# Optimization experiments

Measured on AMD Instinct MI355X. Metric: run time of the kernel, lower is better.

## Reference

```python
import jax, jax.numpy as jnp
import numpy as np
import math

GROUPS = 32
EPS = 1e-5

def group_norm(x, w, b):
    B, C, H, W = x.shape
    xg = x.reshape(B, GROUPS, C // GROUPS, H, W)
    mu = xg.mean(axis=(2, 3, 4), keepdims=True)
    var = xg.var(axis=(2, 3, 4), keepdims=True)
    xn = ((xg - mu) * jax.lax.rsqrt(var + EPS)).reshape(B, C, H, W)
    return xn * w[None, :, None, None] + b[None, :, None, None]

def conv1x1(x, w, b):
    # x: [B,Cin,H,W], w: [Cout,Cin], b: [Cout]
    return jnp.einsum('bchw,oc->bohw', x, w) + b[None, :, None, None]

def setup_inputs() -> dict:
    key = jax.random.key(0)
    ks = jax.random.split(key, 8)
    B, C, E, H, W = 8, 256, 512, 64, 64
    x = jax.random.normal(ks[0], (B, C, H, W), dtype=jnp.float32)
    condA = jax.random.normal(ks[1], (B, E, H, W), dtype=jnp.float32)
    gn_x_w = jnp.ones((C,), jnp.float32)
    gn_x_b = jnp.zeros((C,), jnp.float32)
    gn_c_w = jnp.ones((E,), jnp.float32)
    gn_c_b = jnp.zeros((E,), jnp.float32)
    q_w = jax.random.normal(ks[2], (C, C), jnp.float32) * 0.02
    q_b = jnp.zeros((C,), jnp.float32)
    k_w = jax.random.normal(ks[3], (C, E), jnp.float32) * 0.02
    k_b = jnp.zeros((C,), jnp.float32)
    v_w = jax.random.normal(ks[4], (C, E), jnp.float32) * 0.02
    v_b = jnp.zeros((C,), jnp.float32)
    return {"x": x, "condA": condA, "gn_x_w": gn_x_w, "gn_x_b": gn_x_b,
            "gn_c_w": gn_c_w, "gn_c_b": gn_c_b, "q_w": q_w, "q_b": q_b,
            "k_w": k_w, "k_b": k_b, "v_w": v_w, "v_b": v_b}

def reference(x, condA, gn_x_w, gn_x_b, gn_c_w, gn_c_b, q_w, q_b, k_w, k_b, v_w, v_b):
    B, C, H, W = x.shape
    scale = math.sqrt(C)
    h = group_norm(x, gn_x_w, gn_x_b)
    h1 = group_norm(condA, gn_c_w, gn_c_b)
    q = conv1x1(h, q_w, q_b)      # [B,C,H,W]
    k = conv1x1(h1, k_w, k_b)     # [B,C,Hc,Wc]
    v = conv1x1(h1, v_w, v_b)     # [B,C,Hc,Wc]
    qf = q.transpose(0, 2, 3, 1).reshape(B, H * W, C)        # [B,N,C]
    kf = k.reshape(B, C, -1)                                  # [B,C,M]
    vf = v.transpose(0, 2, 3, 1).reshape(B, -1, C)            # [B,M,C]
    attn = jax.nn.softmax(jnp.einsum('bnc,bcm->bnm', qf, kf) / scale, axis=-1)
    out = jnp.einsum('bnm,bmc->bnc', attn, vf)                # [B,N,C]
    return out.reshape(B, H, W, C).transpose(0, 3, 1, 2)
```

## Files before the change

### kernel.cpp

```cpp
#include <hip/hip_runtime.h>


typedef _Float16 half8 __attribute__((ext_vector_type(8)));
typedef _Float16 half4v __attribute__((ext_vector_type(4)));
typedef float f32x4 __attribute__((ext_vector_type(4)));
typedef float f32x16 __attribute__((ext_vector_type(16)));

#define MFMA16(a, b, c) __builtin_amdgcn_mfma_f32_16x16x32_f16((a), (b), (c), 0, 0, 0)
#define MFMA32(a, b, c) __builtin_amdgcn_mfma_f32_32x32x16_f16((a), (b), (c), 0, 0, 0)

__global__ __launch_bounds__(256) void statswconv_kernel(
    const float* __restrict__ x, const float* __restrict__ condA,
    float* __restrict__ sx, float* __restrict__ sc,
    const float* __restrict__ wq, const float* __restrict__ wk,
    const float* __restrict__ wv, _Float16* __restrict__ wqt,
    _Float16* __restrict__ wkt, _Float16* __restrict__ wvt) {
  int bid = blockIdx.x;
  int t = threadIdx.x;
  if (bid >= 512) {
    int i = (bid - 512) * 256 + t;
    const float* src;
    _Float16* dst;
    int cin, ksbits, gi;
    if (i < 8192) { src = wq; dst = wqt; cin = 256; ksbits = 3; gi = i; }
    else if (i < 24576) { src = wk; dst = wkt; cin = 512; ksbits = 4; gi = i - 8192; }
    else { src = wv; dst = wvt; cin = 512; ksbits = 4; gi = i - 24576; }
    int tile = gi >> 6, g = gi & 63;
    int otile = tile >> ksbits, ks = tile & ((1 << ksbits) - 1);
    int o = otile * 16 + (g & 15), k = ks * 32 + (g >> 4) * 8;
    const float* s = src + (size_t)o * cin + k;
    half8 hv;
#pragma unroll
    for (int j = 0; j < 8; j++) hv[j] = (_Float16)s[j];
    *(half8*)(dst + (size_t)gi * 8) = hv;
    return;
  }
  const float4* src;
  int nf4;
  float* dst;
  float inv_n;
  if (bid < 256) {
    src = (const float4*)(x + (size_t)bid * 32768);
    nf4 = 8192;
    dst = sx + bid * 2;
    inv_n = 1.0f / 32768.0f;
  } else {
    int j = bid - 256;
    src = (const float4*)(condA + (size_t)j * 65536);
    nf4 = 16384;
    dst = sc + j * 2;
    inv_n = 1.0f / 65536.0f;
  }
  float s = 0.f, s2 = 0.f;
  for (int i = t; i < nf4; i += 256) {
    float4 v = src[i];
    s += v.x + v.y + v.z + v.w;
    s2 += v.x * v.x + v.y * v.y + v.z * v.z + v.w * v.w;
  }
#pragma unroll
  for (int m = 1; m <= 32; m <<= 1) {
    s += __shfl_xor(s, m, 64);
    s2 += __shfl_xor(s2, m, 64);
  }
  __shared__ float red[8];
  int w = t >> 6;
  if ((t & 63) == 0) { red[w * 2] = s; red[w * 2 + 1] = s2; }
  __syncthreads();
  if (t == 0) {
    float S = red[0] + red[2] + red[4] + red[6];
    float S2 = red[1] + red[3] + red[5] + red[7];
    float mu = S * inv_n;
    float var = S2 * inv_n - mu * mu;
    dst[0] = mu;
    dst[1] = rsqrtf(var + 1e-5f);
  }
}

__global__ __launch_bounds__(256) void ntrans_kernel(
    const float* __restrict__ x, const float* __restrict__ condA,
    const float* __restrict__ statsx, const float* __restrict__ statsc,
    const float* __restrict__ gxw, const float* __restrict__ gxb,
    const float* __restrict__ gcw, const float* __restrict__ gcb,
    _Float16* __restrict__ hxTt, _Float16* __restrict__ h1Tt) {
  int bid = blockIdx.x;
  const float *src, *stats, *gw, *gb;
  _Float16* dst;
  int CH, gsh, bid2;
  if (bid < 2048) {
    src = x; stats = statsx; gw = gxw; gb = gxb; dst = hxTt;
    CH = 256; gsh = 3; bid2 = bid;
  } else {
    src = condA; stats = statsc; gw = gcw; gb = gcb; dst = h1Tt;
    CH = 512; gsh = 4; bid2 = bid - 2048;
  }
  int b = bid2 & 7, nt = (bid2 >> 3) & 63, ctile = bid2 >> 9;
  int n0 = nt * 64, c0 = ctile * 64;
  int t = threadIdx.x;
  __shared__ float tile[64][65];

  int cl = t >> 2;
  int c = c0 + cl;
  const float* st = stats + ((size_t)b * 32 + (c >> gsh)) * 2;
  float mu = st[0], rs = st[1];
  float a = rs * gw[c];
  float bb = gb[c] - mu * a;
  const float* srow = src + ((size_t)(b * CH + c)) * 4096 + n0 + (t & 3) * 16;
#pragma unroll
  for (int i = 0; i < 4; i++) {
    float4 v = *(const float4*)(srow + 4 * i);
    int nn = (t & 3) * 16 + 4 * i;
    tile[cl][nn + 0] = v.x * a + bb;
    tile[cl][nn + 1] = v.y * a + bb;
    tile[cl][nn + 2] = v.z * a + bb;
    tile[cl][nn + 3] = v.w * a + bb;
  }
  __syncthreads();
  int nl = t >> 2;
  half8 ov[2];
#pragma unroll
  for (int u = 0; u < 2; u++)
#pragma unroll
    for (int i = 0; i < 8; i++) ov[u][i] = (_Float16)tile[(t & 3) * 16 + 8 * u + i][nl];
  int n = n0 + nl;
  size_t tb = ((size_t)b * 256 + (n >> 4)) * (CH >> 5);
  int ca = c0 + (t & 3) * 16;
#pragma unroll
  for (int u = 0; u < 2; u++) {
    int cc = ca + 8 * u;
    size_t addr = ((tb + (cc >> 5)) * 64 + (n & 15) + 16 * ((cc >> 3) & 3)) * 8;
    *(half8*)(dst + addr) = ov[u];
  }
}

__global__ __launch_bounds__(256, 2) void projQ_kernel(
    const _Float16* __restrict__ Ht, const _Float16* __restrict__ Wt,
    const float* __restrict__ bias, _Float16* __restrict__ Qt) {
  int bid = blockIdx.x;
  int b = bid & 7, nt = bid >> 3;
  int t = threadIdx.x, l = t & 63, w = t >> 6;
  int c15 = l & 15, q = l >> 4;

  __shared__ __align__(16) _Float16 hbuf[16384];
  half8* hb = (half8*)hbuf;
  {
    const half8* sg = (const half8*)Ht + (size_t)(b * 256 + nt * 4) * 512;
#pragma unroll
    for (int i = 0; i < 8; i++) hb[t + 256 * i] = sg[t + 256 * i];
  }
  __syncthreads();

  const half8* wt8 = (const half8*)Wt;
#pragma unroll
  for (int p = 0; p < 2; p++) {
    int oa = (p * 4 + w) * 2;
    f32x4 acc[2][4] = {};
#pragma unroll
    for (int ks = 0; ks < 8; ks++) {
      half8 af0 = wt8[((size_t)(oa + 0) * 8 + ks) * 64 + l];
      half8 af1 = wt8[((size_t)(oa + 1) * 8 + ks) * 64 + l];
#pragma unroll
      for (int nt2 = 0; nt2 < 4; nt2++) {
        half8 bf = hb[(nt2 * 8 + ks) * 64 + l];
        acc[0][nt2] = MFMA16(af0, bf, acc[0][nt2]);
        acc[1][nt2] = MFMA16(af1, bf, acc[1][nt2]);
      }
    }
#pragma unroll
    for (int j = 0; j < 2; j++) {
      int o4 = (oa + j) * 16 + 4 * q;
      f32x4 bv = *(const f32x4*)(bias + o4);
#pragma unroll
      for (int nt2 = 0; nt2 < 4; nt2++) {
        half4v hv;
#pragma unroll
        for (int r = 0; r < 4; r++) hv[r] = (_Float16)((acc[j][nt2][r] + bv[r]) * 0.0625f);
        size_t addr = ((((size_t)b * 128 + nt * 2 + (nt2 >> 1)) * 16 + (oa + j)) * 64 +
                       (nt2 & 1) * 16 + c15 + 32 * (q >> 1)) * 8 + (q & 1) * 4;
        *(half4v*)(Qt + addr) = hv;
      }
    }
  }
}

__global__ __launch_bounds__(256, 2) void projKV_kernel(
    const _Float16* __restrict__ Ht, const _Float16* __restrict__ Wk,
    const _Float16* __restrict__ Wv, const float* __restrict__ kb,
    const float* __restrict__ vb, _Float16* __restrict__ Kt,
    _Float16* __restrict__ Vt) {
  int bid = blockIdx.x;
  int b = bid & 7, mt = bid >> 3;
  int m0 = mt * 64;
  int t = threadIdx.x, l = t & 63, w = t >> 6;
  int c15 = l & 15, q = l >> 4;

  __shared__ __align__(16) _Float16 hbuf[32768];
  half8* hb = (half8*)hbuf;
  {
    const half8* sg = (const half8*)Ht + (size_t)(b * 256 + mt * 4) * 1024;
#pragma unroll
    for (int i = 0; i < 16; i++) hb[t + 256 * i] = sg[t + 256 * i];
  }
  __syncthreads();

  const half8* wk8 = (const half8*)Wk;
  const half8* wv8 = (const half8*)Wv;
#pragma unroll
  for (int p = 0; p < 2; p++) {
    int oa = (p * 4 + w) * 2;
    f32x4 acck[2][4] = {};
    f32x4 accv[4][2] = {};
#pragma unroll
    for (int ks = 0; ks < 16; ks++) {
      half8 kf0 = wk8[((size_t)(oa + 0) * 16 + ks) * 64 + l];
      half8 kf1 = wk8[((size_t)(oa + 1) * 16 + ks) * 64 + l];
      half8 vf0 = wv8[((size_t)(oa + 0) * 16 + ks) * 64 + l];
      half8 vf1 = wv8[((size_t)(oa + 1) * 16 + ks) * 64 + l];
#pragma unroll
      for (int nt2 = 0; nt2 < 4; nt2++) {
        half8 lf = hb[(nt2 * 16 + ks) * 64 + l];
        acck[0][nt2] = MFMA16(kf0, lf, acck[0][nt2]);
        acck[1][nt2] = MFMA16(kf1, lf, acck[1][nt2]);
        accv[nt2][0] = MFMA16(lf, vf0, accv[nt2][0]);
        accv[nt2][1] = MFMA16(lf, vf1, accv[nt2][1]);
      }
    }
#pragma unroll
    for (int j = 0; j < 2; j++) {
      int o4 = (oa + j) * 16 + 4 * q;
      f32x4 bv = *(const f32x4*)(kb + o4);
#pragma unroll
      for (int nt2 = 0; nt2 < 4; nt2++) {
        half4v hv;
#pragma unroll
        for (int r = 0; r < 4; r++) hv[r] = (_Float16)(acck[j][nt2][r] + bv[r]);
        size_t addr = ((((size_t)b * 128 + mt * 2 + (nt2 >> 1)) * 16 + (oa + j)) * 64 +
                       (nt2 & 1) * 16 + c15 + 32 * (q >> 1)) * 8 + (q & 1) * 4;
        *(half4v*)(Kt + addr) = hv;
      }
    }
#pragma unroll
    for (int nt2 = 0; nt2 < 4; nt2++) {
      int m = m0 + nt2 * 16 + 4 * q;
      size_t mbase = ((size_t)b * 256 + (m >> 4)) * 8;
#pragma unroll
      for (int j = 0; j < 2; j++) {
        int c = (oa + j) * 16 + c15;
        float bs = vb[c];
        half4v hv;
#pragma unroll
        for (int r = 0; r < 4; r++) hv[r] = (_Float16)(accv[nt2][j][r] + bs);
        size_t addr = ((mbase + (c >> 5)) * 64 + (c & 31) + ((q >> 1) << 5)) * 8 + (q & 1) * 4;
        *(half4v*)(Vt + addr) = hv;
      }
    }
  }
}

__global__ __launch_bounds__(256, 2) void attn_kernel(
    const _Float16* __restrict__ Qt, const _Float16* __restrict__ Kt,
    const _Float16* __restrict__ Vt, float* __restrict__ out) {
  int bid = blockIdx.x;
  int b = bid & 7, nt = bid >> 3;
  int n0 = nt * 64;
  int t = threadIdx.x, l = t & 63, w = t >> 6;
  int l31 = l & 31, h = l >> 5;
  int mh = w & 1, nh = w >> 1;

  __shared__ __align__(16) _Float16 kbuf[16384];
  __shared__ __align__(16) _Float16 pbuf[4096];
  __shared__ float lsw[2][64];
  half8* kb8 = (half8*)kbuf;

  half8 qf[16];
  {
    const half8* qt8 = (const half8*)Qt + ((size_t)(b * 128 + nt * 2 + nh) * 16) * 64 + l;
#pragma unroll
    for (int ks = 0; ks < 16; ks++) qf[ks] = qt8[ks * 64];
  }

  const half8* ktb = (const half8*)Kt + (size_t)b * 131072 + t;
  const half8* vt8 = (const half8*)Vt + (size_t)b * 256 * 8 * 64;
  int gb = (l31 ^ h) | (h << 5);

  f32x16 acc_o[4] = {};
  float l_part = 0.f;

  half8 kreg[8];
#pragma unroll
  for (int i = 0; i < 8; i++) kreg[i] = ktb[256 * i];
#pragma unroll
  for (int i = 0; i < 8; i++) kb8[t + 256 * i] = kreg[i];
  __syncthreads();

  for (int it = 0; it < 64; it++) {
    int itn = it < 63 ? it + 1 : 63;
#pragma unroll
    for (int i = 0; i < 8; i++) kreg[i] = ktb[itn * 2048 + 256 * i];
    half8 vf0[8];
#pragma unroll
    for (int u = 0; u < 2; u++)
#pragma unroll
      for (int ct = 0; ct < 4; ct++)
        vf0[u * 4 + ct] = vt8[((size_t)(it * 4 + u) * 8 + (mh * 4 + ct)) * 64 + l];

    f32x16 s = {};
#pragma unroll
    for (int ks = 0; ks < 16; ks++) {
      half8 kf = kb8[(mh * 16 + ks) * 64 + l];
      s = MFMA32(kf, qf[ks], s);
    }

    half4v pv[4];
#pragma unroll
    for (int k2 = 0; k2 < 4; k2++) {
#pragma unroll
      for (int r = 0; r < 4; r++) {
        float e = __expf(s[4 * k2 + r]);
        l_part += e;
        pv[k2][r] = (_Float16)e;
      }
    }
    __syncthreads();

#pragma unroll
    for (int k2 = 0; k2 < 4; k2++) {
      int hm = k2 & 1;
      int tau = nh * 4 + mh * 2 + (k2 >> 1);
      int g = (l31 ^ hm) | (hm << 5);
      *(half4v*)&pbuf[tau * 512 + g * 8 + 4 * h] = pv[k2];
    }
#pragma unroll
    for (int i = 0; i < 8; i++) kb8[t + 256 * i] = kreg[i];
    __syncthreads();

    half8 vf1[8];
#pragma unroll
    for (int u = 0; u < 2; u++)
#pragma unroll
      for (int ct = 0; ct < 4; ct++)
        vf1[u * 4 + ct] = vt8[((size_t)(it * 4 + 2 + u) * 8 + (mh * 4 + ct)) * 64 + l];
#pragma unroll
    for (int ks = 0; ks < 2; ks++) {
      half8 pf = *(const half8*)&pbuf[(nh * 4 + ks) * 512 + gb * 8];
#pragma unroll
      for (int ct = 0; ct < 4; ct++) acc_o[ct] = MFMA32(pf, vf0[ks * 4 + ct], acc_o[ct]);
    }
#pragma unroll
    for (int ks = 2; ks < 4; ks++) {
      half8 pf = *(const half8*)&pbuf[(nh * 4 + ks) * 512 + gb * 8];
#pragma unroll
      for (int ct = 0; ct < 4; ct++) acc_o[ct] = MFMA32(pf, vf1[(ks - 2) * 4 + ct], acc_o[ct]);
    }
  }

  {
    float v = l_part + __shfl_xor(l_part, 32, 64);
    if (l < 32) lsw[mh][nh * 32 + l] = v;
  }
  __syncthreads();
#pragma unroll
  for (int k2 = 0; k2 < 4; k2++) {
    int nb = nh * 32 + 4 * h + 8 * k2;
    f32x4 s0 = *(const f32x4*)&lsw[0][nb];
    f32x4 s1 = *(const f32x4*)&lsw[1][nb];
    f32x4 linv;
#pragma unroll
    for (int r = 0; r < 4; r++) linv[r] = 1.0f / (s0[r] + s1[r]);
#pragma unroll
    for (int ct = 0; ct < 4; ct++) {
      int c = mh * 128 + ct * 32 + l31;
      f32x4 o4;
#pragma unroll
      for (int r = 0; r < 4; r++) o4[r] = acc_o[ct][4 * k2 + r] * linv[r];
      *(f32x4*)(out + ((size_t)(b * 256 + c)) * 4096 + n0 + nb) = o4;
    }
  }
}

extern "C" void kernel_launch(void* const* d_in, const int* in_sizes, int n_in,
                              void* d_out, int out_size, void* d_ws,
                              size_t ws_size, hipStream_t stream) {
  const float* x = (const float*)d_in[0];
  const float* condA = (const float*)d_in[1];
  const float* gxw = (const float*)d_in[2];
  const float* gxb = (const float*)d_in[3];
  const float* gcw = (const float*)d_in[4];
  const float* gcb = (const float*)d_in[5];
  const float* qw = (const float*)d_in[6];
  const float* qb = (const float*)d_in[7];
  const float* kw = (const float*)d_in[8];
  const float* kb = (const float*)d_in[9];
  const float* vw = (const float*)d_in[10];
  const float* vb = (const float*)d_in[11];
  float* out = (float*)d_out;

  char* ws = (char*)d_ws;
  float* statsx = (float*)(ws);
  float* statsc = (float*)(ws + 2048);
  _Float16* wqt = (_Float16*)(ws + 4096);
  _Float16* wkt = (_Float16*)(ws + 135168);
  _Float16* wvt = (_Float16*)(ws + 397312);
  char* p = ws + 659456;
  _Float16* hxTt = (_Float16*)p; p += (size_t)8 * 4096 * 256 * 2;
  _Float16* h1Tt = (_Float16*)p; p += (size_t)8 * 4096 * 512 * 2;
  _Float16* Qt = (_Float16*)p;   p += (size_t)8 * 4096 * 256 * 2;
  _Float16* Kt = (_Float16*)p;   p += (size_t)8 * 4096 * 256 * 2;
  _Float16* Vt = (_Float16*)p;

  statswconv_kernel<<<672, 256, 0, stream>>>(x, condA, statsx, statsc,
                                             qw, kw, vw, wqt, wkt, wvt);
  ntrans_kernel<<<6144, 256, 0, stream>>>(x, condA, statsx, statsc,
                                          gxw, gxb, gcw, gcb, hxTt, h1Tt);
  projQ_kernel<<<512, 256, 0, stream>>>(hxTt, wqt, qb, Qt);
  projKV_kernel<<<512, 256, 0, stream>>>(h1Tt, wkt, wvt, kb, vb, Kt, Vt);
  attn_kernel<<<512, 256, 0, stream>>>(Qt, Kt, Vt, out);
}
```

Baseline: 392.9 us.

## Split attention key range across two blocks and add a combine kernel

The attention kernel now splits the 4096 keys into two halves, so the grid grows from 512 to 1024 blocks. Each block writes unnormalized partial outputs and per-row softmax denominators, and a new combine kernel sums the two halves and divides. The goal is to fill the GPU better, since 512 blocks gave only two per CU; launch bounds are also raised to 4 blocks per CU. In exchange it adds partial-output writes, a combine pass that reads and writes again, and a risk of register spilling under the tighter register budget. The partials reuse workspace that the projection kernels have already consumed.

After: 1.224 ms. 211% more time.

```diff
diff --git a/kernel.cpp b/kernel.cpp
--- a/kernel.cpp
+++ b/kernel.cpp
@@ -256,19 +256,22 @@
   }
 }
 
-__global__ __launch_bounds__(256, 2) void attn_kernel(
+__global__ __launch_bounds__(256, 4) void attn_kernel(
     const _Float16* __restrict__ Qt, const _Float16* __restrict__ Kt,
-    const _Float16* __restrict__ Vt, float* __restrict__ out) {
+    const _Float16* __restrict__ Vt, float* __restrict__ out,
+    float* __restrict__ O1, float* __restrict__ l0g,
+    float* __restrict__ l1g) {
   int bid = blockIdx.x;
-  int b = bid & 7, nt = bid >> 3;
+  int b = bid & 7, nt = (bid >> 3) & 63, ms = bid >> 9;
   int n0 = nt * 64;
   int t = threadIdx.x, l = t & 63, w = t >> 6;
   int l31 = l & 31, h = l >> 5;
   int mh = w & 1, nh = w >> 1;
+  int it0 = ms * 32, it1 = it0 + 32;
 
   __shared__ __align__(16) _Float16 kbuf[16384];
   __shared__ __align__(16) _Float16 pbuf[4096];
-  __shared__ float lsw[2][64];
+  float* lsw = (float*)pbuf;
   half8* kb8 = (half8*)kbuf;
 
   half8 qf[16];
@@ -287,13 +290,13 @@
 
   half8 kreg[8];
 #pragma unroll
-  for (int i = 0; i < 8; i++) kreg[i] = ktb[256 * i];
+  for (int i = 0; i < 8; i++) kreg[i] = ktb[it0 * 2048 + 256 * i];
 #pragma unroll
   for (int i = 0; i < 8; i++) kb8[t + 256 * i] = kreg[i];
   __syncthreads();
 
-  for (int it = 0; it < 64; it++) {
-    int itn = it < 63 ? it + 1 : 63;
+  for (int it = it0; it < it1; it++) {
+    int itn = it + 1 < it1 ? it + 1 : it1 - 1;
 #pragma unroll
     for (int i = 0; i < 8; i++) kreg[i] = ktb[itn * 2048 + 256 * i];
     half8 vf0[8];
@@ -353,28 +356,45 @@
     }
   }
 
+  __syncthreads();
   {
     float v = l_part + __shfl_xor(l_part, 32, 64);
-    if (l < 32) lsw[mh][nh * 32 + l] = v;
-  }
-  __syncthreads();
+    if (l < 32) lsw[mh * 64 + nh * 32 + l] = v;
+  }
+  __syncthreads();
+  float* obase = ms ? O1 : out;
 #pragma unroll
   for (int k2 = 0; k2 < 4; k2++) {
     int nb = nh * 32 + 4 * h + 8 * k2;
-    f32x4 s0 = *(const f32x4*)&lsw[0][nb];
-    f32x4 s1 = *(const f32x4*)&lsw[1][nb];
-    f32x4 linv;
-#pragma unroll
-    for (int r = 0; r < 4; r++) linv[r] = 1.0f / (s0[r] + s1[r]);
 #pragma unroll
     for (int ct = 0; ct < 4; ct++) {
       int c = mh * 128 + ct * 32 + l31;
       f32x4 o4;
 #pragma unroll
-      for (int r = 0; r < 4; r++) o4[r] = acc_o[ct][4 * k2 + r] * linv[r];
-      *(f32x4*)(out + ((size_t)(b * 256 + c)) * 4096 + n0 + nb) = o4;
-    }
-  }
+      for (int r = 0; r < 4; r++) o4[r] = acc_o[ct][4 * k2 + r];
+      *(f32x4*)(obase + ((size_t)(b * 256 + c)) * 4096 + n0 + nb) = o4;
+    }
+  }
+  if (t < 64) {
+    float* lG = ms ? l1g : l0g;
+    lG[b * 4096 + n0 + t] = lsw[t] + lsw[64 + t];
+  }
+}
+
+__global__ __launch_bounds__(256) void combine_kernel(
+    float* __restrict__ out, const float* __restrict__ O1,
+    const float* __restrict__ l0g, const float* __restrict__ l1g) {
+  size_t i = (size_t)blockIdx.x * 256 + threadIdx.x;
+  f32x4 a = ((const f32x4*)out)[i];
+  f32x4 b4 = ((const f32x4*)O1)[i];
+  int bidx = (int)(i >> 18);
+  int n4 = (int)(i & 1023);
+  f32x4 La = ((const f32x4*)l0g)[bidx * 1024 + n4];
+  f32x4 Lb = ((const f32x4*)l1g)[bidx * 1024 + n4];
+  f32x4 r;
+#pragma unroll
+  for (int j = 0; j < 4; j++) r[j] = (a[j] + b4[j]) / (La[j] + Lb[j]);
+  ((f32x4*)out)[i] = r;
 }
 
 extern "C" void kernel_launch(void* const* d_in, const int* in_sizes, int n_in,
@@ -407,11 +427,16 @@
   _Float16* Kt = (_Float16*)p;   p += (size_t)8 * 4096 * 256 * 2;
   _Float16* Vt = (_Float16*)p;
 
+  float* O1 = (float*)(ws + 659456);
+  float* l0g = (float*)(ws + 659456 + (size_t)33554432);
+  float* l1g = (float*)(ws + 659456 + (size_t)33554432 + 131072);
+
   statswconv_kernel<<<672, 256, 0, stream>>>(x, condA, statsx, statsc,
                                              qw, kw, vw, wqt, wkt, wvt);
   ntrans_kernel<<<6144, 256, 0, stream>>>(x, condA, statsx, statsc,
                                           gxw, gxb, gcw, gcb, hxTt, h1Tt);
   projQ_kernel<<<512, 256, 0, stream>>>(hxTt, wqt, qb, Qt);
   projKV_kernel<<<512, 256, 0, stream>>>(h1Tt, wkt, wvt, kb, vb, Kt, Vt);
-  attn_kernel<<<512, 256, 0, stream>>>(Qt, Kt, Vt, out);
-}
+  attn_kernel<<<1024, 256, 0, stream>>>(Qt, Kt, Vt, out, O1, l0g, l1g);
+  combine_kernel<<<8192, 256, 0, stream>>>(out, O1, l0g, l1g);
+}
```
